# Kernel optimization log

Measured on AMD Instinct MI355X. Metric: run time of the kernel, lower is better.

Reference implementation:

```python
import jax, jax.numpy as jnp
import numpy as np

B, A, N, D = 512, 3, 64, 32


def _lte(x):
    """LTETransform: straight-through hard threshold (forward: 1[x>0], backward: identity)."""
    hard = (x > 0).astype(x.dtype)
    return x + jax.lax.stop_gradient(hard - x)


def setup_inputs() -> dict:
    key = jax.random.key(0)
    k1, k2 = jax.random.split(key)
    feature = jax.random.normal(k1, (B, N, D), dtype=jnp.float32)
    indicator = jax.random.normal(k2, (A, N, D), dtype=jnp.float32)
    return {"feature": feature, "indicator": indicator}


def reference(feature, indicator):
    # gate = LTE(DotWeight(indicator[0], indicator[1])) -> [N, N]
    gate = _lte(jnp.einsum('id,jd->ij', indicator[0], indicator[1]))

    # QKV[a,i,j,:,:] = indicator[a,i,:] (outer) indicator[a,j,:]  (rank-1), so
    # input[b,a,i,j,d] = (feature[b,i,:] . indicator[a,i,:]) * indicator[a,j,d]
    s = jnp.einsum('bnd,and->ban', feature, indicator)  # [B, 3, N]

    # query[b,i,j,d] = elu(s[b,0,i] * ind[0,j,d]) + 1              [B,N,N,D]
    q = jax.nn.elu(s[:, 0, :, None, None] * indicator[0][None, None, :, :]) + 1.0
    # key.transpose(1,2)[b,i,j,d] = elu(s[b,1,j] * ind[1,i,d]) + 1  [B,N,N,D]
    k_t = jax.nn.elu(s[:, 1, None, :, None] * indicator[1][None, :, None, :]) + 1.0

    score = jnp.einsum('bijd,bijd->bij', q, k_t)  # [B, N, N]
    probs = jax.nn.softmax(score, axis=-1)
    score_hat = probs * gate[None, :, :]

    # value[b,i,j,d] = s[b,2,i] * ind[2,j,d];  out = sum_j scoreHat * value
    out = s[:, 2, :, None] * jnp.einsum('bij,jd->bid', score_hat, indicator[2])
    return out  # [B, N, D]
```

## Files before the change

### kernel.cpp

```cpp
#include <hip/hip_runtime.h>

namespace {
constexpr int N   = 64;
constexpr int D   = 32;
constexpr int PD  = 36;
constexpr int SHP = 104;
constexpr float LOG2E = 1.4426950408889634f;
constexpr float LN2   = 0.6931471805599453f;

typedef float f32x2 __attribute__((ext_vector_type(2)));

#if __has_builtin(__builtin_amdgcn_exp2f)
__device__ __forceinline__ float fexp2(float x) { return __builtin_amdgcn_exp2f(x); }
#else
__device__ __forceinline__ float fexp2(float x) { return exp2f(x); }
#endif
#if __has_builtin(__builtin_amdgcn_rcpf)
__device__ __forceinline__ float frcp(float x) { return __builtin_amdgcn_rcpf(x); }
#else
__device__ __forceinline__ float frcp(float x) { return 1.0f / x; }
#endif
__device__ __forceinline__ void wavebar() {
#if __has_builtin(__builtin_amdgcn_wave_barrier)
    __builtin_amdgcn_wave_barrier();
#endif
}

__global__ __launch_bounds__(512, 4) void fused(
        const float* __restrict__ feature,
        const float* __restrict__ ind,
        float* __restrict__ out) {
    __shared__ float ind_lds[3][N][PD];
    __shared__ float s_lds[3][N];
    __shared__ float sh_lds[32][SHP];

    const int t      = threadIdx.x;
    const int lane   = t & 63;
    const int wave   = t >> 6;
    const int blk    = blockIdx.x;
    const int b      = blk >> 1;
    const int i_base = (blk & 1) << 5;

    {
        const float4* src = reinterpret_cast<const float4*>(ind);
#pragma unroll
        for (int idx = t; idx < 3 * N * D / 4; idx += 512) {
            int a = idx >> 9;
            int r = idx & 511;
            int n = r >> 3;
            int k = r & 7;
            *reinterpret_cast<float4*>(&ind_lds[a][n][k * 4]) = src[idx];
        }
    }

    if (t < 3 * N) {
        int a = t >> 6, n = t & 63;
        const float4* frow = reinterpret_cast<const float4*>(feature + ((size_t)b * N + n) * D);
        const float4* irow = reinterpret_cast<const float4*>(ind + (a * N + n) * D);
        f32x2 sa2 = {0.f, 0.f};
#pragma unroll
        for (int k = 0; k < 8; ++k) {
            float4 f4 = frow[k];
            float4 i4 = irow[k];
            sa2 = __builtin_elementwise_fma(f32x2{f4.x, f4.y}, f32x2{i4.x, i4.y}, sa2);
            sa2 = __builtin_elementwise_fma(f32x2{f4.z, f4.w}, f32x2{i4.z, i4.w}, sa2);
        }
        s_lds[a][n] = sa2.x + sa2.y;
    }
    __syncthreads();

    int igu[4];
#pragma unroll
    for (int r = 0; r < 4; ++r)
        igu[r] = __builtin_amdgcn_readfirstlane(i_base + wave * 4 + r);

    unsigned long long gmask[4];
    {
        f32x2 ga[4] = {{0.f, 0.f}, {0.f, 0.f}, {0.f, 0.f}, {0.f, 0.f}};
#pragma unroll
        for (int k = 0; k < 8; ++k) {
            float4 w4 = *reinterpret_cast<const float4*>(&ind_lds[1][lane][k * 4]);
            f32x2 wp0 = {w4.x, w4.y}, wp1 = {w4.z, w4.w};
#pragma unroll
            for (int r = 0; r < 4; ++r) {
                float4 a4 = *reinterpret_cast<const float4*>(ind + igu[r] * D + k * 4);
                ga[r] = __builtin_elementwise_fma(f32x2{a4.x, a4.y}, wp0, ga[r]);
                ga[r] = __builtin_elementwise_fma(f32x2{a4.z, a4.w}, wp1, ga[r]);
            }
        }
#pragma unroll
        for (int r = 0; r < 4; ++r) gmask[r] = __ballot(ga[r].x + ga[r].y > 0.f);
    }

    const float s1Ls = s_lds[1][lane] * LOG2E;
    const f32x2 s1L  = {s1Ls, s1Ls};
    const f32x2 ln2v = {LN2, LN2};
    const f32x2 onev = {1.0f, 1.0f};
    const f32x2 zerv = {0.0f, 0.0f};

    float s0v[4];
#pragma unroll
    for (int r = 0; r < 4; ++r) s0v[r] = s_lds[0][i_base + wave * 4 + r] * LOG2E;

    f32x2 sc2[4] = {{0.f, 0.f}, {0.f, 0.f}, {0.f, 0.f}, {0.f, 0.f}};

#define SCORE_BODY(NEGA, FMAA, AM, FM)                                              \
    {                                                                               \
        const f32x2 amv = {(AM), (AM)};                                             \
        const f32x2 fmv = {(FM), (FM)};                                             \
        f32x2 acc = sc2[r];                                                         \
        _Pragma("unroll")                                                           \
        for (int k4 = 0; k4 < 4; ++k4) {                                            \
            float4 v4 = *reinterpret_cast<const float4*>(                           \
                ind + N * D + igu[r] * D + c * 16 + k4 * 4);            \
            f32x2 vp[2] = {f32x2{v4.x, v4.y}, f32x2{v4.z, v4.w}};                   \
            _Pragma("unroll")                                                       \
            for (int h = 0; h < 2; ++h) {                                           \
                f32x2 aneg = amv * NEGA[k4 * 2 + h];                                \
                f32x2 A    = __builtin_elementwise_fma(fmv, FMAA[k4 * 2 + h], onev);\
                f32x2 bL   = s1L * vp[h];                                           \
                f32x2 bneg = __builtin_elementwise_min(bL, zerv);                   \
                f32x2 B    = __builtin_elementwise_fma(                             \
                    __builtin_elementwise_max(bL, zerv), ln2v, onev);               \
                f32x2 mn   = aneg + bneg;                                           \
                f32x2 E    = {fexp2(mn.x), fexp2(mn.y)};                            \
                acc = __builtin_elementwise_fma(E * A, B, acc);                     \
            }                                                                       \
        }                                                                           \
        sc2[r] = acc;                                                               \
    }

#pragma unroll
    for (int c = 0; c < 2; ++c) {
        f32x2 un[8], upl[8];
#pragma unroll
        for (int k4 = 0; k4 < 4; ++k4) {
            float4 v = *reinterpret_cast<const float4*>(&ind_lds[0][lane][c * 16 + k4 * 4]);
            f32x2 x0 = {v.x, v.y}, x1 = {v.z, v.w};
            f32x2 n0 = __builtin_elementwise_min(x0, zerv);
            f32x2 n1 = __builtin_elementwise_min(x1, zerv);
            un[k4 * 2 + 0]  = n0;
            un[k4 * 2 + 1]  = n1;
            upl[k4 * 2 + 0] = (x0 - n0) * ln2v;
            upl[k4 * 2 + 1] = (x1 - n1) * ln2v;
        }
#pragma unroll
        for (int r = 0; r < 4; ++r) {
            const float s0u = __uint_as_float(
                __builtin_amdgcn_readfirstlane(__float_as_uint(s0v[r])));
            if (s0u >= 0.f) {
                SCORE_BODY(un, upl, s0u, s0u)
            } else {
                SCORE_BODY(upl, un, s0u * LOG2E, s0u * LN2)
            }
        }
    }
#undef SCORE_BODY

    float score[4];
#pragma unroll
    for (int r = 0; r < 4; ++r) score[r] = sc2[r].x + sc2[r].y;

    float mx[4], e[4], sm[4];
#pragma unroll
    for (int r = 0; r < 4; ++r) mx[r] = score[r];
#pragma unroll
    for (int off = 32; off >= 1; off >>= 1) {
#pragma unroll
        for (int r = 0; r < 4; ++r) mx[r] = fmaxf(mx[r], __shfl_xor(mx[r], off));
    }
#pragma unroll
    for (int r = 0; r < 4; ++r) e[r] = fexp2((score[r] - mx[r]) * LOG2E);
#pragma unroll
    for (int r = 0; r < 4; ++r) sm[r] = e[r];
#pragma unroll
    for (int off = 32; off >= 1; off >>= 1) {
#pragma unroll
        for (int r = 0; r < 4; ++r) sm[r] += __shfl_xor(sm[r], off);
    }
#pragma unroll
    for (int r = 0; r < 4; ++r) {
        const int ig    = i_base + wave * 4 + r;
        const int i_loc = wave * 4 + r;
        const float g   = (float)((gmask[r] >> lane) & 1ull);
        sh_lds[i_loc][lane] = (e[r] * g) * (s_lds[2][ig] * frcp(sm[r]));
    }

    wavebar();

    {
        const int i_loc = t >> 4;
        const int sub   = t & 15;
        const int dq    = sub & 7;
        const int jh    = sub >> 3;
        f32x2 acc0 = {0.f, 0.f}, acc1 = {0.f, 0.f};
#pragma unroll
        for (int jj = 0; jj < 32; jj += 4) {
            int j = jh * 32 + jj;
            float4 sh4 = *reinterpret_cast<const float4*>(&sh_lds[i_loc][j]);
#pragma unroll
            for (int c = 0; c < 4; ++c) {
                float4 v4 = *reinterpret_cast<const float4*>(&ind_lds[2][j + c][dq * 4]);
                float  w  = (&sh4.x)[c];
                f32x2 wv = {w, w};
                acc0 = __builtin_elementwise_fma(wv, f32x2{v4.x, v4.y}, acc0);
                acc1 = __builtin_elementwise_fma(wv, f32x2{v4.z, v4.w}, acc1);
            }
        }
        float4 acc = {acc0.x, acc0.y, acc1.x, acc1.y};
        acc.x += __shfl_xor(acc.x, 8);
        acc.y += __shfl_xor(acc.y, 8);
        acc.z += __shfl_xor(acc.z, 8);
        acc.w += __shfl_xor(acc.w, 8);
        if (jh == 0) {
            *reinterpret_cast<float4*>(out + ((size_t)b * N + i_base + i_loc) * D + dq * 4) = acc;
        }
    }
}
}

extern "C" void kernel_launch(void* const* d_in, const int* in_sizes, int n_in,
                              void* d_out, int out_size, void* d_ws, size_t ws_size,
                              hipStream_t stream) {
    const float* feature = (const float*)d_in[0];
    const float* ind     = (const float*)d_in[1];
    float*       out     = (float*)d_out;
    fused<<<1024, 512, 0, stream>>>(feature, ind, out);
}
```

Baseline: 79.91 us.

## Process one full batch per block with eight rows per wave

Each block now handles all 64 query rows of one batch instead of half, so the grid shrinks from 1024 to 512 blocks and every wave computes 8 rows instead of 4. This halves the redundant per-block work of staging the indicator tensor into shared memory and computing the s projections, which were repeated for both halves of a batch. The output stage drops the split-j reduction across lanes, so each thread accumulates all 64 j terms and writes directly. The cost is more registers per wave, which may reduce occupancy under the launch bound, and fewer blocks to spread across compute units.

```diff
diff --git a/kernel.cpp b/kernel.cpp
--- a/kernel.cpp
+++ b/kernel.cpp
@@ -4,7 +4,7 @@
 constexpr int N   = 64;
 constexpr int D   = 32;
 constexpr int PD  = 36;
-constexpr int SHP = 104;
+constexpr int SHP = 72;
 constexpr float LOG2E = 1.4426950408889634f;
 constexpr float LN2   = 0.6931471805599453f;
 
@@ -32,14 +32,12 @@
         float* __restrict__ out) {
     __shared__ float ind_lds[3][N][PD];
     __shared__ float s_lds[3][N];
-    __shared__ float sh_lds[32][SHP];
-
-    const int t      = threadIdx.x;
-    const int lane   = t & 63;
-    const int wave   = t >> 6;
-    const int blk    = blockIdx.x;
-    const int b      = blk >> 1;
-    const int i_base = (blk & 1) << 5;
+    __shared__ float sh_lds[N][SHP];
+
+    const int t    = threadIdx.x;
+    const int lane = t & 63;
+    const int wave = t >> 6;
+    const int b    = blockIdx.x;
 
     {
         const float4* src = reinterpret_cast<const float4*>(ind);
@@ -69,27 +67,31 @@
     }
     __syncthreads();
 
-    int igu[4];
-#pragma unroll
-    for (int r = 0; r < 4; ++r)
-        igu[r] = __builtin_amdgcn_readfirstlane(i_base + wave * 4 + r);
-
-    unsigned long long gmask[4];
+    int igu[8];
+#pragma unroll
+    for (int r = 0; r < 8; ++r)
+        igu[r] = __builtin_amdgcn_readfirstlane(wave * 8 + r);
+
+    unsigned long long gmask[8];
     {
-        f32x2 ga[4] = {{0.f, 0.f}, {0.f, 0.f}, {0.f, 0.f}, {0.f, 0.f}};
-#pragma unroll
-        for (int k = 0; k < 8; ++k) {
-            float4 w4 = *reinterpret_cast<const float4*>(&ind_lds[1][lane][k * 4]);
-            f32x2 wp0 = {w4.x, w4.y}, wp1 = {w4.z, w4.w};
-#pragma unroll
-            for (int r = 0; r < 4; ++r) {
-                float4 a4 = *reinterpret_cast<const float4*>(ind + igu[r] * D + k * 4);
-                ga[r] = __builtin_elementwise_fma(f32x2{a4.x, a4.y}, wp0, ga[r]);
-                ga[r] = __builtin_elementwise_fma(f32x2{a4.z, a4.w}, wp1, ga[r]);
+        f32x2 wv[16];
+#pragma unroll
+        for (int k4 = 0; k4 < 8; ++k4) {
+            float4 w4 = *reinterpret_cast<const float4*>(&ind_lds[1][lane][k4 * 4]);
+            wv[k4 * 2 + 0] = f32x2{w4.x, w4.y};
+            wv[k4 * 2 + 1] = f32x2{w4.z, w4.w};
+        }
+#pragma unroll
+        for (int r = 0; r < 8; ++r) {
+            f32x2 ga = {0.f, 0.f};
+#pragma unroll
+            for (int k4 = 0; k4 < 8; ++k4) {
+                float4 a4 = *reinterpret_cast<const float4*>(ind + igu[r] * D + k4 * 4);
+                ga = __builtin_elementwise_fma(f32x2{a4.x, a4.y}, wv[k4 * 2 + 0], ga);
+                ga = __builtin_elementwise_fma(f32x2{a4.z, a4.w}, wv[k4 * 2 + 1], ga);
             }
-        }
-#pragma unroll
-        for (int r = 0; r < 4; ++r) gmask[r] = __ballot(ga[r].x + ga[r].y > 0.f);
+            gmask[r] = __ballot(ga.x + ga.y > 0.f);
+        }
     }
 
     const float s1Ls = s_lds[1][lane] * LOG2E;
@@ -98,11 +100,12 @@
     const f32x2 onev = {1.0f, 1.0f};
     const f32x2 zerv = {0.0f, 0.0f};
 
-    float s0v[4];
-#pragma unroll
-    for (int r = 0; r < 4; ++r) s0v[r] = s_lds[0][i_base + wave * 4 + r] * LOG2E;
-
-    f32x2 sc2[4] = {{0.f, 0.f}, {0.f, 0.f}, {0.f, 0.f}, {0.f, 0.f}};
+    float s0v[8];
+#pragma unroll
+    for (int r = 0; r < 8; ++r) s0v[r] = s_lds[0][wave * 8 + r] * LOG2E;
+
+    f32x2 sc2[8] = {{0.f, 0.f}, {0.f, 0.f}, {0.f, 0.f}, {0.f, 0.f},
+                    {0.f, 0.f}, {0.f, 0.f}, {0.f, 0.f}, {0.f, 0.f}};
 
 #define SCORE_BODY(NEGA, FMAA, AM, FM)                                              \
     {                                                                               \
@@ -145,7 +148,7 @@
             upl[k4 * 2 + 1] = (x1 - n1) * ln2v;
         }
 #pragma unroll
-        for (int r = 0; r < 4; ++r) {
+        for (int r = 0; r < 8; ++r) {
             const float s0u = __uint_as_float(
                 __builtin_amdgcn_readfirstlane(__float_as_uint(s0v[r])));
             if (s0u >= 0.f) {
@@ -157,64 +160,54 @@
     }
 #undef SCORE_BODY
 
-    float score[4];
-#pragma unroll
-    for (int r = 0; r < 4; ++r) score[r] = sc2[r].x + sc2[r].y;
-
-    float mx[4], e[4], sm[4];
-#pragma unroll
-    for (int r = 0; r < 4; ++r) mx[r] = score[r];
+    float score[8];
+#pragma unroll
+    for (int r = 0; r < 8; ++r) score[r] = sc2[r].x + sc2[r].y;
+
+    float mx[8], e[8], sm[8];
+#pragma unroll
+    for (int r = 0; r < 8; ++r) mx[r] = score[r];
 #pragma unroll
     for (int off = 32; off >= 1; off >>= 1) {
 #pragma unroll
-        for (int r = 0; r < 4; ++r) mx[r] = fmaxf(mx[r], __shfl_xor(mx[r], off));
-    }
-#pragma unroll
-    for (int r = 0; r < 4; ++r) e[r] = fexp2((score[r] - mx[r]) * LOG2E);
-#pragma unroll
-    for (int r = 0; r < 4; ++r) sm[r] = e[r];
+        for (int r = 0; r < 8; ++r) mx[r] = fmaxf(mx[r], __shfl_xor(mx[r], off));
+    }
+#pragma unroll
+    for (int r = 0; r < 8; ++r) e[r] = fexp2((score[r] - mx[r]) * LOG2E);
+#pragma unroll
+    for (int r = 0; r < 8; ++r) sm[r] = e[r];
 #pragma unroll
     for (int off = 32; off >= 1; off >>= 1) {
 #pragma unroll
-        for (int r = 0; r < 4; ++r) sm[r] += __shfl_xor(sm[r], off);
-    }
-#pragma unroll
-    for (int r = 0; r < 4; ++r) {
-        const int ig    = i_base + wave * 4 + r;
-        const int i_loc = wave * 4 + r;
-        const float g   = (float)((gmask[r] >> lane) & 1ull);
-        sh_lds[i_loc][lane] = (e[r] * g) * (s_lds[2][ig] * frcp(sm[r]));
+        for (int r = 0; r < 8; ++r) sm[r] += __shfl_xor(sm[r], off);
+    }
+#pragma unroll
+    for (int r = 0; r < 8; ++r) {
+        const int ig  = wave * 8 + r;
+        const float g = (float)((gmask[r] >> lane) & 1ull);
+        sh_lds[ig][lane] = (e[r] * g) * (s_lds[2][ig] * frcp(sm[r]));
     }
 
     wavebar();
 
     {
-        const int i_loc = t >> 4;
-        const int sub   = t & 15;
-        const int dq    = sub & 7;
-        const int jh    = sub >> 3;
+        const int i_loc = t >> 3;
+        const int dq    = t & 7;
         f32x2 acc0 = {0.f, 0.f}, acc1 = {0.f, 0.f};
 #pragma unroll
-        for (int jj = 0; jj < 32; jj += 4) {
-            int j = jh * 32 + jj;
+        for (int j = 0; j < 64; j += 4) {
             float4 sh4 = *reinterpret_cast<const float4*>(&sh_lds[i_loc][j]);
 #pragma unroll
             for (int c = 0; c < 4; ++c) {
                 float4 v4 = *reinterpret_cast<const float4*>(&ind_lds[2][j + c][dq * 4]);
                 float  w  = (&sh4.x)[c];
-                f32x2 wv = {w, w};
-                acc0 = __builtin_elementwise_fma(wv, f32x2{v4.x, v4.y}, acc0);
-                acc1 = __builtin_elementwise_fma(wv, f32x2{v4.z, v4.w}, acc1);
+                f32x2 wvv = {w, w};
+                acc0 = __builtin_elementwise_fma(wvv, f32x2{v4.x, v4.y}, acc0);
+                acc1 = __builtin_elementwise_fma(wvv, f32x2{v4.z, v4.w}, acc1);
             }
         }
         float4 acc = {acc0.x, acc0.y, acc1.x, acc1.y};
-        acc.x += __shfl_xor(acc.x, 8);
-        acc.y += __shfl_xor(acc.y, 8);
-        acc.z += __shfl_xor(acc.z, 8);
-        acc.w += __shfl_xor(acc.w, 8);
-        if (jh == 0) {
-            *reinterpret_cast<float4*>(out + ((size_t)b * N + i_base + i_loc) * D + dq * 4) = acc;
-        }
+        *reinterpret_cast<float4*>(out + ((size_t)b * N + i_loc) * D + dq * 4) = acc;
     }
 }
 }
@@ -225,5 +218,5 @@
     const float* feature = (const float*)d_in[0];
     const float* ind     = (const float*)d_in[1];
     float*       out     = (float*)d_out;
-    fused<<<1024, 512, 0, stream>>>(feature, ind, out);
-}
+    fused<<<512, 512, 0, stream>>>(feature, ind, out);
+}
```

New measurement: 79.53 us. No clear change (-0.5%).

## Raise occupancy target and shrink register live ranges in score loop

Applied to the files above, without the earlier changes.

Doubles the launch_bounds minimum blocks per CU from 4 to 8 and reduces the shared-memory row pitch of sh_lds so more blocks can be resident. To fit the tighter register budget, the gate dot-product is reordered to keep one accumulator live at a time, and the score loop splits D into four chunks of 8 instead of two of 16, halving the un/upl register arrays. The readfirstlane of s0 is hoisted out of the chunk loop. Forcing the higher occupancy risks register spills, and if SHP is smaller than the column range the softmax writes use, shared-memory rows could overlap.

```diff
diff --git a/kernel.cpp b/kernel.cpp
--- a/kernel.cpp
+++ b/kernel.cpp
@@ -4,7 +4,7 @@
 constexpr int N   = 64;
 constexpr int D   = 32;
 constexpr int PD  = 36;
-constexpr int SHP = 104;
+constexpr int SHP = 72;
 constexpr float LOG2E = 1.4426950408889634f;
 constexpr float LN2   = 0.6931471805599453f;
 
@@ -26,7 +26,7 @@
 #endif
 }
 
-__global__ __launch_bounds__(512, 4) void fused(
+__global__ __launch_bounds__(512, 8) void fused(
         const float* __restrict__ feature,
         const float* __restrict__ ind,
         float* __restrict__ out) {
@@ -76,20 +76,24 @@
 
     unsigned long long gmask[4];
     {
-        f32x2 ga[4] = {{0.f, 0.f}, {0.f, 0.f}, {0.f, 0.f}, {0.f, 0.f}};
-#pragma unroll
-        for (int k = 0; k < 8; ++k) {
-            float4 w4 = *reinterpret_cast<const float4*>(&ind_lds[1][lane][k * 4]);
-            f32x2 wp0 = {w4.x, w4.y}, wp1 = {w4.z, w4.w};
-#pragma unroll
-            for (int r = 0; r < 4; ++r) {
-                float4 a4 = *reinterpret_cast<const float4*>(ind + igu[r] * D + k * 4);
-                ga[r] = __builtin_elementwise_fma(f32x2{a4.x, a4.y}, wp0, ga[r]);
-                ga[r] = __builtin_elementwise_fma(f32x2{a4.z, a4.w}, wp1, ga[r]);
+        f32x2 wv[16];
+#pragma unroll
+        for (int k4 = 0; k4 < 8; ++k4) {
+            float4 w4 = *reinterpret_cast<const float4*>(&ind_lds[1][lane][k4 * 4]);
+            wv[k4 * 2 + 0] = f32x2{w4.x, w4.y};
+            wv[k4 * 2 + 1] = f32x2{w4.z, w4.w};
+        }
+#pragma unroll
+        for (int r = 0; r < 4; ++r) {
+            f32x2 ga = {0.f, 0.f};
+#pragma unroll
+            for (int k4 = 0; k4 < 8; ++k4) {
+                float4 a4 = *reinterpret_cast<const float4*>(ind + igu[r] * D + k4 * 4);
+                ga = __builtin_elementwise_fma(f32x2{a4.x, a4.y}, wv[k4 * 2 + 0], ga);
+                ga = __builtin_elementwise_fma(f32x2{a4.z, a4.w}, wv[k4 * 2 + 1], ga);
             }
-        }
-#pragma unroll
-        for (int r = 0; r < 4; ++r) gmask[r] = __ballot(ga[r].x + ga[r].y > 0.f);
+            gmask[r] = __ballot(ga.x + ga.y > 0.f);
+        }
     }
 
     const float s1Ls = s_lds[1][lane] * LOG2E;
@@ -98,9 +102,11 @@
     const f32x2 onev = {1.0f, 1.0f};
     const f32x2 zerv = {0.0f, 0.0f};
 
-    float s0v[4];
-#pragma unroll
-    for (int r = 0; r < 4; ++r) s0v[r] = s_lds[0][i_base + wave * 4 + r] * LOG2E;
+    float s0u[4];
+#pragma unroll
+    for (int r = 0; r < 4; ++r)
+        s0u[r] = __uint_as_float(__builtin_amdgcn_readfirstlane(
+            __float_as_uint(s_lds[0][i_base + wave * 4 + r] * LOG2E)));
 
     f32x2 sc2[4] = {{0.f, 0.f}, {0.f, 0.f}, {0.f, 0.f}, {0.f, 0.f}};
 
@@ -110,9 +116,9 @@
         const f32x2 fmv = {(FM), (FM)};                                             \
         f32x2 acc = sc2[r];                                                         \
         _Pragma("unroll")                                                           \
-        for (int k4 = 0; k4 < 4; ++k4) {                                            \
+        for (int k4 = 0; k4 < 2; ++k4) {                                            \
             float4 v4 = *reinterpret_cast<const float4*>(                           \
-                ind + N * D + igu[r] * D + c * 16 + k4 * 4);            \
+                ind + N * D + igu[r] * D + c * 8 + k4 * 4);             \
             f32x2 vp[2] = {f32x2{v4.x, v4.y}, f32x2{v4.z, v4.w}};                   \
             _Pragma("unroll")                                                       \
             for (int h = 0; h < 2; ++h) {                                           \
@@ -131,11 +137,11 @@
     }
 
 #pragma unroll
-    for (int c = 0; c < 2; ++c) {
-        f32x2 un[8], upl[8];
-#pragma unroll
-        for (int k4 = 0; k4 < 4; ++k4) {
-            float4 v = *reinterpret_cast<const float4*>(&ind_lds[0][lane][c * 16 + k4 * 4]);
+    for (int c = 0; c < 4; ++c) {
+        f32x2 un[4], upl[4];
+#pragma unroll
+        for (int k4 = 0; k4 < 2; ++k4) {
+            float4 v = *reinterpret_cast<const float4*>(&ind_lds[0][lane][c * 8 + k4 * 4]);
             f32x2 x0 = {v.x, v.y}, x1 = {v.z, v.w};
             f32x2 n0 = __builtin_elementwise_min(x0, zerv);
             f32x2 n1 = __builtin_elementwise_min(x1, zerv);
@@ -146,12 +152,10 @@
         }
 #pragma unroll
         for (int r = 0; r < 4; ++r) {
-            const float s0u = __uint_as_float(
-                __builtin_amdgcn_readfirstlane(__float_as_uint(s0v[r])));
-            if (s0u >= 0.f) {
-                SCORE_BODY(un, upl, s0u, s0u)
+            if (s0u[r] >= 0.f) {
+                SCORE_BODY(un, upl, s0u[r], s0u[r])
             } else {
-                SCORE_BODY(upl, un, s0u * LOG2E, s0u * LN2)
+                SCORE_BODY(upl, un, s0u[r] * LOG2E, s0u[r] * LN2)
             }
         }
     }
@@ -202,9 +206,9 @@
             for (int c = 0; c < 4; ++c) {
                 float4 v4 = *reinterpret_cast<const float4*>(&ind_lds[2][j + c][dq * 4]);
                 float  w  = (&sh4.x)[c];
-                f32x2 wv = {w, w};
-                acc0 = __builtin_elementwise_fma(wv, f32x2{v4.x, v4.y}, acc0);
-                acc1 = __builtin_elementwise_fma(wv, f32x2{v4.z, v4.w}, acc1);
+                f32x2 wvv = {w, w};
+                acc0 = __builtin_elementwise_fma(wvv, f32x2{v4.x, v4.y}, acc0);
+                acc1 = __builtin_elementwise_fma(wvv, f32x2{v4.z, v4.w}, acc1);
             }
         }
         float4 acc = {acc0.x, acc0.y, acc1.x, acc1.y};
```

Result: no change. 81.42 us (+1.9%).
